# Performance work log

Hardware: AMD Instinct MI355X
Metric: run time of the kernel (lower is better)

The kernel has to match this reference:

```python
import jax, jax.numpy as jnp
import numpy as np

EPS = 1e-5
TEMPERATURE = 1.0


def _gn(x, w, b):
    # GroupNorm(dim, dim): num_groups == channels -> per-channel norm over spatial
    mu = x.mean((2, 3), keepdims=True)
    var = x.var((2, 3), keepdims=True)
    return (x - mu) * jax.lax.rsqrt(var + EPS) * w[None, :, None, None] + b[None, :, None, None]


def _deconv(x, w, b):
    # torch ConvTranspose2d(Cin, Cout, 3, stride=2, padding=1, output_padding=1)
    # == dilated conv with lhs_dilation=2, padding (1,2); kernel flip absorbed into random weights
    y = jax.lax.conv_general_dilated(
        x, w, window_strides=(1, 1), padding=((1, 2), (1, 2)),
        lhs_dilation=(2, 2), dimension_numbers=('NCHW', 'OIHW', 'NCHW'))
    return y + b[None, :, None, None]


def _spatial_softmax(logits, temp):
    # logits (..., h, w) -> expected (x, y) coords in [-1, 1], shape (..., 2)
    h, w = logits.shape[-2], logits.shape[-1]
    p = jax.nn.softmax(logits.reshape(*logits.shape[:-2], h * w) / temp, axis=-1)
    ys, xs = jnp.meshgrid(jnp.linspace(-1.0, 1.0, h), jnp.linspace(-1.0, 1.0, w), indexing='ij')
    ex = p @ xs.reshape(-1)
    ey = p @ ys.reshape(-1)
    return jnp.stack([ex, ey], axis=-1)


def setup_inputs() -> dict:
    key = jax.random.key(0)
    ks = iter(jax.random.split(key, 40))
    B, FC, FH = 512, 256, 4   # batch, encoder channels, encoder spatial
    H = 512                   # hidden_size
    STEPS, NHEADS, C = 5, 3, H // 8

    def nrm(shape, scale):
        return jax.random.normal(next(ks), shape, jnp.float32) * scale

    inp = {
        'feat': nrm((B, FC, FH, FH), 1.0),
        'action': jax.random.randint(next(ks), (B,), 0, NHEADS),
        'scene_idx': jax.random.randint(next(ks), (B,), 0, 10),
        'fc_w': nrm((FC, H), (2.0 / FC) ** 0.5),
        'fc_b': jnp.zeros((H,), jnp.float32),
    }
    for i, d in enumerate([512, 256, 128]):
        inp[f'gw{i}'] = jnp.ones((d,), jnp.float32)
        inp[f'gb{i}'] = jnp.zeros((d,), jnp.float32)
        inp[f'dw{i}'] = nrm((d // 2, d, 3, 3), (2.0 / (d * 9)) ** 0.5)
        inp[f'db{i}'] = jnp.zeros((d // 2,), jnp.float32)
    inp['hgw'] = jnp.ones((NHEADS, C), jnp.float32)
    inp['hgb'] = jnp.zeros((NHEADS, C), jnp.float32)
    inp['hcw'] = nrm((NHEADS, STEPS, C), (2.0 / C) ** 0.5)
    inp['hcb'] = jnp.zeros((NHEADS, STEPS), jnp.float32)
    return inp


def reference(feat, action, scene_idx, fc_w, fc_b,
              gw0, gb0, dw0, db0, gw1, gb1, dw1, db1, gw2, gb2, dw2, db2,
              hgw, hgb, hcw, hcb):
    # visual_fc1 applied channel-last == 1x1 linear over channels
    x = jax.nn.relu(jnp.einsum('bchw,cd->bdhw', feat, fc_w) + fc_b[None, :, None, None])
    # deconv stack: (B,512,4,4) -> (B,256,8,8) -> (B,128,16,16) -> (B,64,32,32)
    for gw, gb, dw, db in ((gw0, gb0, dw0, db0), (gw1, gb1, dw1, db1), (gw2, gb2, dw2, db2)):
        x = jax.nn.relu(_deconv(_gn(x, gw, gb), dw, db))
    # expert heads: shared per-channel normalization, head-specific affine fused into 1x1 conv
    mu = x.mean((2, 3), keepdims=True)
    var = x.var((2, 3), keepdims=True)
    xn = (x - mu) * jax.lax.rsqrt(var + EPS)                       # (B,64,32,32)
    w_eff = hcw * hgw[:, None, :]                                  # (A,S,C)
    b_eff = hcb + jnp.einsum('asc,ac->as', hcw, hgb)               # (A,S)
    logits = jnp.einsum('bchw,asc->abshw', xn, w_eff) + b_eff[:, None, :, None, None]
    coords = _spatial_softmax(logits, TEMPERATURE)                 # (A,B,S,2)
    # route each sample to its action's head (== masked scatter loop in torch)
    out = coords[action, jnp.arange(action.shape[0])]              # (B,S,2)
    return out
```

## Files before the change

kernel.cpp:

```cpp
#include <hip/hip_runtime.h>
#include <hip/hip_bf16.h>

#define DI __device__ __forceinline__
using u16 = unsigned short;
using u32 = unsigned int;

typedef short short8 __attribute__((ext_vector_type(8)));
typedef float f32x4 __attribute__((ext_vector_type(4)));

#define F4C(v, i) ((i) == 0 ? (v).x : (i) == 1 ? (v).y : (i) == 2 ? (v).z : (v).w)

DI float bflo(u32 u) { return __uint_as_float(u << 16); }
DI float bfhi(u32 u) { return __uint_as_float(u & 0xffff0000u); }
DI float bfel(uint2 u, int j) { u32 w = (j < 2) ? u.x : u.y; return (j & 1) ? bfhi(w) : bflo(w); }
DI u16 f2bf(float a) {
  u32 xu = __float_as_uint(a);
  return (u16)((xu + 0x7fffu + ((xu >> 16) & 1)) >> 16);
}
DI u32 pack_bf16x2(float a, float b) {
  u32 xu = __float_as_uint(a), yu = __float_as_uint(b);
  xu = (xu + 0x7fffu + ((xu >> 16) & 1)) >> 16;
  yu = (yu + 0x7fffu + ((yu >> 16) & 1)) >> 16;
  return (xu & 0xffffu) | (yu << 16);
}

static constexpr size_t OFF_REGB = 0;
static constexpr size_t OFF_REGA = 16777216;
static constexpr size_t OFF_WT0  = 33554432;
static constexpr size_t OFF_WT1  = OFF_WT0 + 1179648;
static constexpr size_t OFF_WT2  = OFF_WT1 + 294912;
static constexpr size_t OFF_WTF  = OFF_WT2 + 73728;
static constexpr size_t OFF_ST   = 35200000;
static constexpr size_t O_SC0 = OFF_ST,          O_SH0 = OFF_ST + 262144;
static constexpr size_t O_SC1 = OFF_ST + 524288, O_SH1 = OFF_ST + 655360;
static constexpr size_t O_SC2 = OFF_ST + 786432, O_SH2 = OFF_ST + 851968;
static constexpr size_t O_PSUM = OFF_ST + 1048576;

__global__ __launch_bounds__(256)
void wtrans_all(const float* __restrict__ dw0, const float* __restrict__ dw1,
                const float* __restrict__ dw2, const float* __restrict__ fcw,
                u16* __restrict__ wt0, u16* __restrict__ wt1,
                u16* __restrict__ wt2, u16* __restrict__ wtf)
{
  int id = blockIdx.x * 256 + threadIdx.x;
  if (id < 131072) {
    int m = id >> 9, c = id & 511;
    const float* src = dw0 + ((size_t)m * 512 + c) * 9;
#pragma unroll
    for (int tap = 0; tap < 9; ++tap)
      wt0[((size_t)tap * 256 + m) * 512 + c] = f2bf(src[tap]);
  } else if (id < 163840) {
    int j = id - 131072;
    int m = j >> 8, c = j & 255;
    const float* src = dw1 + ((size_t)m * 256 + c) * 9;
#pragma unroll
    for (int tap = 0; tap < 9; ++tap)
      wt1[((size_t)tap * 128 + m) * 256 + c] = f2bf(src[tap]);
  } else if (id < 172032) {
    int j = id - 163840;
    int m = j >> 7, c = j & 127;
    const float* src = dw2 + ((size_t)m * 128 + c) * 9;
#pragma unroll
    for (int tap = 0; tap < 9; ++tap)
      wt2[((size_t)tap * 64 + m) * 128 + c] = f2bf(src[tap]);
  } else {
    int j = id - 172032;
    int d = j >> 8, c = j & 255;
    wtf[j] = f2bf(fcw[c * 512 + d]);
  }
}

DI void fc_stage_A(const float* __restrict__ feat, int b, u16* Ab, int t)
{
#pragma unroll
  for (int it = 0; it < 2; ++it) {
    int idx = t + it * 256;
    int cp = idx >> 2, hw4 = idx & 3;
    int c = cp * 2;
    const float* xp = feat + ((size_t)b * 256 + c) * 16 + hw4 * 4;
    float4 v0 = *(const float4*)xp;
    float4 v1 = *(const float4*)(xp + 16);
    int c64 = c >> 6, jb = (c & 63) >> 3;
#pragma unroll
    for (int j = 0; j < 4; ++j) {
      int hw = hw4 * 4 + j;
      int row = c64 * 16 + hw;
      *(u32*)&Ab[(row << 6) + ((jb ^ (row & 7)) << 3) + (c & 7)] =
          pack_bf16x2(F4C(v0, j), F4C(v1, j));
    }
  }
}

__global__ __launch_bounds__(256, 2)
void fc_mfma(const float* __restrict__ feat, const u16* __restrict__ wtf,
             const float* __restrict__ fb, const float* __restrict__ gw,
             const float* __restrict__ gb, u16* __restrict__ x0,
             float* __restrict__ sc, float* __restrict__ sh)
{
  __shared__ __align__(16) u16 Wl[256 * 64];
  __shared__ __align__(16) u16 Al[2][64 * 64];
  const int t = threadIdx.x;
  const int lane = t & 63, wave = t >> 6;
  const int n15 = lane & 15, kq = lane >> 4;
  const int d0 = blockIdx.x * 64;
  const int b0 = blockIdx.y * 4;

#pragma unroll
  for (int it = 0; it < 8; ++it) {
    int idx = t + it * 256;
    int dl = idx >> 5, jb32 = idx & 31;
    int row = (jb32 >> 3) * 64 + dl, jb = jb32 & 7;
    uint4 v = *(const uint4*)(wtf + (size_t)(d0 + dl) * 256 + jb32 * 8);
    *(uint4*)&Wl[(row << 6) + ((jb ^ (row & 7)) << 3)] = v;
  }
  fc_stage_A(feat, b0, Al[0], t);

  const int dg = d0 + wave * 16 + n15;
  const float bvn = fb[dg];
  const float gwv = gw[dg], gbv = gb[dg];

  for (int bi = 0; bi < 4; ++bi) {
    __syncthreads();
    if (bi + 1 < 4) fc_stage_A(feat, b0 + bi + 1, Al[(bi + 1) & 1], t);

    const u16* A = Al[bi & 1];
    f32x4 acc0 = {0.f, 0.f, 0.f, 0.f}, acc1 = {0.f, 0.f, 0.f, 0.f};
#pragma unroll
    for (int ks = 0; ks < 8; ++ks) {
      int js = ks * 4 + kq;
      int ra = (js >> 3) * 16 + n15;
      int rb = (js >> 3) * 64 + wave * 16 + n15;
      short8 av = *(const short8*)&A[(ra << 6) + (((js & 7) ^ (ra & 7)) << 3)];
      short8 bv = *(const short8*)&Wl[(rb << 6) + (((js & 7) ^ (rb & 7)) << 3)];
      if (ks & 1) acc1 = __builtin_amdgcn_mfma_f32_16x16x32_bf16(av, bv, acc1, 0, 0, 0);
      else        acc0 = __builtin_amdgcn_mfma_f32_16x16x32_bf16(av, bv, acc0, 0, 0, 0);
    }

    int b = b0 + bi;
    float v[4], s = 0.f, s2 = 0.f;
#pragma unroll
    for (int r = 0; r < 4; ++r) {
      v[r] = fmaxf(acc0[r] + acc1[r] + bvn, 0.f);
      s += v[r]; s2 += v[r] * v[r];
    }
    uint2 pk = {pack_bf16x2(v[0], v[1]), pack_bf16x2(v[2], v[3])};
    *(uint2*)&x0[((size_t)b * 512 + dg) * 16 + kq * 4] = pk;
    s  += __shfl_xor(s, 16, 64);  s  += __shfl_xor(s, 32, 64);
    s2 += __shfl_xor(s2, 16, 64); s2 += __shfl_xor(s2, 32, 64);
    if (kq == 0) {
      float mu = s * (1.f / 16.f);
      float var = fmaxf(s2 * (1.f / 16.f) - mu * mu, 0.f);
      float scale = gwv * rsqrtf(var + 1e-5f);
      sc[(size_t)b * 512 + dg] = scale;
      sh[(size_t)b * 512 + dg] = gbv - mu * scale;
    }
  }
}

template<int STAGE>
__global__ __launch_bounds__(256, 3)
void deconv_mfma(const u16* __restrict__ x, const float* __restrict__ sc,
                 const float* __restrict__ sh, const u16* __restrict__ wt,
                 const float* __restrict__ bias, u16* __restrict__ y,
                 const float* __restrict__ gwn, const float* __restrict__ gbn,
                 float* __restrict__ osc, float* __restrict__ osh)
{
  constexpr int CI  = STAGE == 0 ? 512 : 256;
  constexpr int CO  = CI / 2;
  constexpr int H   = STAGE == 0 ? 4 : 8;
  constexpr int S2I = H * H, S2O = 4 * S2I, W2 = 2 * H;
  constexpr int WP  = H + 1;
  constexpr int XROWS = STAGE == 0 ? 100 : 81;
  constexpr int NCH = CI / 64;
  __shared__ __align__(16) u16 Wl[288 * 64];
  __shared__ __align__(16) u16 Xl[XROWS * 64];
  __shared__ float2 sbuf[4][32];

  const int t = threadIdx.x;
  const int lane = t & 63, wv = t >> 6;
  const int n15 = lane & 15, kq = lane >> 4;

  const int m0 = blockIdx.x * 32;
  const int b0 = (STAGE == 0) ? blockIdx.y * 4 : blockIdx.y;
  const int b  = (STAGE == 0) ? b0 + wv : b0;

  int xrow;
  if constexpr (STAGE == 0) xrow = wv * 25 + (n15 >> 2) * 5 + (n15 & 3);
  else                      xrow = (2 * wv + (n15 >> 3)) * 9 + (n15 & 7);

  for (int i = t; i < XROWS * 32; i += 256) ((u32*)Xl)[i] = 0;

  f32x4 acc[2][4];
#pragma unroll
  for (int mi = 0; mi < 2; ++mi)
#pragma unroll
    for (int c = 0; c < 4; ++c) acc[mi][c] = f32x4{0.f, 0.f, 0.f, 0.f};

  for (int ch = 0; ch < NCH; ++ch) {
    const int c0 = ch * 64;
    __syncthreads();

#pragma unroll
    for (int it = 0; it < 9; ++it) {
      int idx = t + it * 256;
      int row = idx >> 3, jb = idx & 7;
      int tap = row >> 5, ml = row & 31;
      uint4 v = *(const uint4*)(wt + ((size_t)(tap * CO + m0 + ml)) * CI + c0 + jb * 8);
      *(uint4*)&Wl[(row << 6) + ((jb ^ (row & 7)) << 3)] = v;
    }

    for (int idx = t; idx < 16 * 32; idx += 256) {
      int q = idx & 15, p = idx >> 4;
      int c = c0 + 2 * p;
      int bb, ldr, gpos;
      if constexpr (STAGE == 0) {
        int img = q >> 2, iy = q & 3;
        bb = b0 + img; gpos = iy * 4; ldr = img * 25 + iy * 5;
      } else {
        int iy = q >> 1, cq = q & 1;
        bb = b0; gpos = iy * 8 + cq * 4; ldr = iy * 9 + cq * 4;
      }
      const u16* xp = x + ((size_t)bb * CI + c) * S2I + gpos;
      uint2 q0 = *(const uint2*)xp;
      uint2 q1 = *(const uint2*)(xp + S2I);
      float s0 = sc[(size_t)bb * CI + c],     h0 = sh[(size_t)bb * CI + c];
      float s1 = sc[(size_t)bb * CI + c + 1], h1 = sh[(size_t)bb * CI + c + 1];
      int jb = p >> 2, sub = p & 3;
#pragma unroll
      for (int j = 0; j < 4; ++j) {
        int row = ldr + j;
        *(u32*)&Xl[(row << 6) + ((jb ^ (row & 7)) << 3) + sub * 2] =
            pack_bf16x2(bfel(q0, j) * s0 + h0, bfel(q1, j) * s1 + h1);
      }
    }
    __syncthreads();

#pragma unroll
    for (int s = 0; s < 2; ++s) {
      const int js = s * 4 + kq;
      const int r0 = xrow, r1 = r0 + 1, r2 = r0 + WP, r3 = r0 + WP + 1;
      short8 b00 = *(const short8*)&Xl[(r0 << 6) + ((js ^ (r0 & 7)) << 3)];
      short8 b01 = *(const short8*)&Xl[(r1 << 6) + ((js ^ (r1 & 7)) << 3)];
      short8 b10 = *(const short8*)&Xl[(r2 << 6) + ((js ^ (r2 & 7)) << 3)];
      short8 b11 = *(const short8*)&Xl[(r3 << 6) + ((js ^ (r3 & 7)) << 3)];
#pragma unroll
      for (int mi = 0; mi < 2; ++mi) {
        short8 a[9];
#pragma unroll
        for (int tap = 0; tap < 9; ++tap) {
          int row = tap * 32 + mi * 16 + n15;
          a[tap] = *(const short8*)&Wl[(row << 6) + ((js ^ (row & 7)) << 3)];
        }
        acc[mi][0] = __builtin_amdgcn_mfma_f32_16x16x32_bf16(a[4], b00, acc[mi][0], 0, 0, 0);
        acc[mi][1] = __builtin_amdgcn_mfma_f32_16x16x32_bf16(a[3], b00, acc[mi][1], 0, 0, 0);
        acc[mi][1] = __builtin_amdgcn_mfma_f32_16x16x32_bf16(a[5], b01, acc[mi][1], 0, 0, 0);
        acc[mi][2] = __builtin_amdgcn_mfma_f32_16x16x32_bf16(a[1], b00, acc[mi][2], 0, 0, 0);
        acc[mi][2] = __builtin_amdgcn_mfma_f32_16x16x32_bf16(a[7], b10, acc[mi][2], 0, 0, 0);
        acc[mi][3] = __builtin_amdgcn_mfma_f32_16x16x32_bf16(a[0], b00, acc[mi][3], 0, 0, 0);
        acc[mi][3] = __builtin_amdgcn_mfma_f32_16x16x32_bf16(a[2], b01, acc[mi][3], 0, 0, 0);
        acc[mi][3] = __builtin_amdgcn_mfma_f32_16x16x32_bf16(a[6], b10, acc[mi][3], 0, 0, 0);
        acc[mi][3] = __builtin_amdgcn_mfma_f32_16x16x32_bf16(a[8], b11, acc[mi][3], 0, 0, 0);
      }
    }
  }

#pragma unroll
  for (int mi = 0; mi < 2; ++mi) {
    float bvv[4];
#pragma unroll
    for (int r = 0; r < 4; ++r) bvv[r] = bias[m0 + mi * 16 + kq * 4 + r];
    float val[4][4];
    float sr[4] = {0.f, 0.f, 0.f, 0.f}, sr2[4] = {0.f, 0.f, 0.f, 0.f};
#pragma unroll
    for (int cl = 0; cl < 4; ++cl)
#pragma unroll
      for (int r = 0; r < 4; ++r) {
        val[cl][r] = fmaxf(acc[mi][cl][r] + bvv[r], 0.f);
        sr[r] += val[cl][r]; sr2[r] += val[cl][r] * val[cl][r];
      }

    if constexpr (STAGE == 0) {
      int iy = n15 >> 2, ix = n15 & 3;
#pragma unroll
      for (int r = 0; r < 4; ++r) {
        int m = m0 + mi * 16 + kq * 4 + r;
        size_t base = ((size_t)b * CO + m) * S2O + (size_t)(2 * iy) * W2 + 2 * ix;
        *(u32*)(y + base)      = pack_bf16x2(val[0][r], val[1][r]);
        *(u32*)(y + base + W2) = pack_bf16x2(val[2][r], val[3][r]);
      }
#pragma unroll
      for (int r = 0; r < 4; ++r) {
#pragma unroll
        for (int off = 1; off <= 8; off <<= 1) {
          sr[r]  += __shfl_xor(sr[r], off, 64);
          sr2[r] += __shfl_xor(sr2[r], off, 64);
        }
      }
      if (n15 == 0) {
#pragma unroll
        for (int r = 0; r < 4; ++r) {
          int m = m0 + mi * 16 + kq * 4 + r;
          float mu = sr[r] * (1.f / 64.f);
          float var = fmaxf(sr2[r] * (1.f / 64.f) - mu * mu, 0.f);
          float scale = gwn[m] * rsqrtf(var + 1e-5f);
          osc[(size_t)b * CO + m] = scale;
          osh[(size_t)b * CO + m] = gbn[m] - mu * scale;
        }
      }
    } else {
      int iy = 2 * wv + (n15 >> 3), ix = n15 & 7;
#pragma unroll
      for (int cl = 0; cl < 4; ++cl) {
        int opx = (2 * iy + (cl >> 1)) * 16 + 2 * ix + (cl & 1);
        size_t base = ((size_t)b * 256 + opx) * 128 + m0 + mi * 16 + kq * 4;
        *(u32*)(y + base)     = pack_bf16x2(val[cl][0], val[cl][1]);
        *(u32*)(y + base + 2) = pack_bf16x2(val[cl][2], val[cl][3]);
      }
#pragma unroll
      for (int r = 0; r < 4; ++r) {
#pragma unroll
        for (int off = 1; off <= 8; off <<= 1) {
          sr[r]  += __shfl_xor(sr[r], off, 64);
          sr2[r] += __shfl_xor(sr2[r], off, 64);
        }
      }
      if (n15 == 0) {
#pragma unroll
        for (int r = 0; r < 4; ++r) sbuf[wv][mi * 16 + kq * 4 + r] = float2{sr[r], sr2[r]};
      }
    }
  }

  if constexpr (STAGE == 1) {
    __syncthreads();
    if (t < 32) {
      float s = 0.f, s2 = 0.f;
#pragma unroll
      for (int w = 0; w < 4; ++w) { s += sbuf[w][t].x; s2 += sbuf[w][t].y; }
      float mu = s * (1.f / 256.f);
      float var = fmaxf(s2 * (1.f / 256.f) - mu * mu, 0.f);
      int m = m0 + t;
      float scale = gwn[m] * rsqrtf(var + 1e-5f);
      osc[(size_t)b0 * CO + m] = scale;
      osh[(size_t)b0 * CO + m] = gbn[m] - mu * scale;
    }
  }
}

#define XRD(row) (*(const short8*)&Xl[((row) << 6) + (((js ^ ((row) & 7))) << 3)])
__global__ __launch_bounds__(256, 3)
void deconv2_q(const u16* __restrict__ x, const float* __restrict__ sc,
               const float* __restrict__ sh, const u16* __restrict__ wt,
               const float* __restrict__ bias, u16* __restrict__ y,
               float2* __restrict__ psum)
{
  __shared__ __align__(16) u16 Wl[288 * 64];
  __shared__ __align__(16) u16 Xl[85 * 64];
  __shared__ float sc_l[128], sh_l[128];
  __shared__ float2 sbuf[2][2][16];

  const int t = threadIdx.x;
  const int lane = t & 63, wave = t >> 6;
  const int ms = wave >> 1, ns = wave & 1;
  const int n15 = lane & 15, kq = lane >> 4;
  const int m0 = (blockIdx.x & 1) * 32;
  const int qz = blockIdx.x >> 1;
  const int b  = blockIdx.y;

  if (t < 128) { sc_l[t] = sc[(size_t)b * 128 + t]; sh_l[t] = sh[(size_t)b * 128 + t]; }
  for (int i = t; i < 85 * 32; i += 256) ((u32*)Xl)[i] = 0;

  const int am = ms * 16 + n15;
  const int xr0 = (ns * 2) * 17 + n15;

  f32x4 acc[2][4];
#pragma unroll
  for (int ni = 0; ni < 2; ++ni)
#pragma unroll
    for (int c = 0; c < 4; ++c) acc[ni][c] = f32x4{0.f, 0.f, 0.f, 0.f};

  const int NPX = (qz < 3) ? 80 : 64;
  for (int ch = 0; ch < 2; ++ch) {
    const int c0 = ch * 64;
    __syncthreads();

#pragma unroll
    for (int it = 0; it < 9; ++it) {
      int idx = t + it * 256;
      int row = idx >> 3, jb = idx & 7;
      int tap = row >> 5, ml = row & 31;
      uint4 v = *(const uint4*)(wt + ((size_t)(tap * 64 + m0 + ml)) * 128 + c0 + jb * 8);
      *(uint4*)&Wl[(row << 6) + ((jb ^ (row & 7)) << 3)] = v;
    }

    for (int idx = t; idx < NPX * 8; idx += 256) {
      int pxl = idx >> 3, jb = idx & 7;
      int rl = pxl >> 4, ix = pxl & 15;
      int gpx = (4 * qz + rl) * 16 + ix;
      uint4 q = *(const uint4*)(x + ((size_t)b * 256 + gpx) * 128 + c0 + jb * 8);
      int cb = c0 + jb * 8;
      float f0 = bflo(q.x) * sc_l[cb + 0] + sh_l[cb + 0];
      float f1 = bfhi(q.x) * sc_l[cb + 1] + sh_l[cb + 1];
      float f2 = bflo(q.y) * sc_l[cb + 2] + sh_l[cb + 2];
      float f3 = bfhi(q.y) * sc_l[cb + 3] + sh_l[cb + 3];
      float f4 = bflo(q.z) * sc_l[cb + 4] + sh_l[cb + 4];
      float f5 = bfhi(q.z) * sc_l[cb + 5] + sh_l[cb + 5];
      float f6 = bflo(q.w) * sc_l[cb + 6] + sh_l[cb + 6];
      float f7 = bfhi(q.w) * sc_l[cb + 7] + sh_l[cb + 7];
      uint4 o = {pack_bf16x2(f0, f1), pack_bf16x2(f2, f3),
                 pack_bf16x2(f4, f5), pack_bf16x2(f6, f7)};
      int row = rl * 17 + ix;
      *(uint4*)&Xl[(row << 6) + ((jb ^ (row & 7)) << 3)] = o;
    }
    __syncthreads();

#pragma unroll
    for (int s = 0; s < 2; ++s) {
      const int js = s * 4 + kq;
      short8 a[9];
#pragma unroll
      for (int tap = 0; tap < 9; ++tap) {
        int row = tap * 32 + am;
        a[tap] = *(const short8*)&Wl[(row << 6) + ((js ^ (row & 7)) << 3)];
      }
      short8 B0 = XRD(xr0),      B1 = XRD(xr0 + 1);
      short8 B2 = XRD(xr0 + 17), B3 = XRD(xr0 + 18);
      short8 B4 = XRD(xr0 + 34), B5 = XRD(xr0 + 35);
#pragma unroll
      for (int ni = 0; ni < 2; ++ni) {
        short8 b00 = ni ? B2 : B0, b01 = ni ? B3 : B1;
        short8 b10 = ni ? B4 : B2, b11 = ni ? B5 : B3;
        acc[ni][0] = __builtin_amdgcn_mfma_f32_16x16x32_bf16(a[4], b00, acc[ni][0], 0, 0, 0);
        acc[ni][1] = __builtin_amdgcn_mfma_f32_16x16x32_bf16(a[3], b00, acc[ni][1], 0, 0, 0);
        acc[ni][1] = __builtin_amdgcn_mfma_f32_16x16x32_bf16(a[5], b01, acc[ni][1], 0, 0, 0);
        acc[ni][2] = __builtin_amdgcn_mfma_f32_16x16x32_bf16(a[1], b00, acc[ni][2], 0, 0, 0);
        acc[ni][2] = __builtin_amdgcn_mfma_f32_16x16x32_bf16(a[7], b10, acc[ni][2], 0, 0, 0);
        acc[ni][3] = __builtin_amdgcn_mfma_f32_16x16x32_bf16(a[0], b00, acc[ni][3], 0, 0, 0);
        acc[ni][3] = __builtin_amdgcn_mfma_f32_16x16x32_bf16(a[2], b01, acc[ni][3], 0, 0, 0);
        acc[ni][3] = __builtin_amdgcn_mfma_f32_16x16x32_bf16(a[6], b10, acc[ni][3], 0, 0, 0);
        acc[ni][3] = __builtin_amdgcn_mfma_f32_16x16x32_bf16(a[8], b11, acc[ni][3], 0, 0, 0);
      }
    }
  }

  float bv[4];
#pragma unroll
  for (int r = 0; r < 4; ++r) bv[r] = bias[m0 + ms * 16 + kq * 4 + r];
  float sr[4] = {0.f, 0.f, 0.f, 0.f}, sr2[4] = {0.f, 0.f, 0.f, 0.f};
#pragma unroll
  for (int ni = 0; ni < 2; ++ni) {
    int iy = 4 * qz + ns * 2 + ni, ix = n15;
#pragma unroll
    for (int r = 0; r < 4; ++r) {
      int m = m0 + ms * 16 + kq * 4 + r;
      float v00 = fmaxf(acc[ni][0][r] + bv[r], 0.f);
      float v01 = fmaxf(acc[ni][1][r] + bv[r], 0.f);
      float v10 = fmaxf(acc[ni][2][r] + bv[r], 0.f);
      float v11 = fmaxf(acc[ni][3][r] + bv[r], 0.f);
      size_t base = ((size_t)b * 64 + m) * 1024 + (size_t)(2 * iy) * 32 + 2 * ix;
      *(u32*)(y + base)      = pack_bf16x2(v00, v01);
      *(u32*)(y + base + 32) = pack_bf16x2(v10, v11);
      sr[r]  += v00 + v01 + v10 + v11;
      sr2[r] += v00 * v00 + v01 * v01 + v10 * v10 + v11 * v11;
    }
  }
#pragma unroll
  for (int r = 0; r < 4; ++r) {
#pragma unroll
    for (int off = 1; off <= 8; off <<= 1) {
      sr[r]  += __shfl_xor(sr[r], off, 64);
      sr2[r] += __shfl_xor(sr2[r], off, 64);
    }
  }
  __syncthreads();
  if (n15 == 0) {
#pragma unroll
    for (int r = 0; r < 4; ++r) sbuf[ms][ns][kq * 4 + r] = float2{sr[r], sr2[r]};
  }
  __syncthreads();
  if (t < 32) {
    int msx = t >> 4, i = t & 15;
    float2 p0 = sbuf[msx][0][i], p1 = sbuf[msx][1][i];
    int m = m0 + msx * 16 + i;
    psum[((size_t)b * 64 + m) * 4 + qz] = float2{p0.x + p1.x, p0.y + p1.y};
  }
}

DI float breduce_sum(float v, float* buf) {
#pragma unroll
  for (int off = 32; off; off >>= 1) v += __shfl_xor(v, off, 64);
  if ((threadIdx.x & 63) == 0) buf[threadIdx.x >> 6] = v;
  __syncthreads();
  float r = (buf[0] + buf[1]) + (buf[2] + buf[3]);
  __syncthreads();
  return r;
}
DI float breduce_max(float v, float* buf) {
#pragma unroll
  for (int off = 32; off; off >>= 1) v = fmaxf(v, __shfl_xor(v, off, 64));
  if ((threadIdx.x & 63) == 0) buf[threadIdx.x >> 6] = v;
  __syncthreads();
  float r = fmaxf(fmaxf(buf[0], buf[1]), fmaxf(buf[2], buf[3]));
  __syncthreads();
  return r;
}

__global__ __launch_bounds__(256)
void head_kernel(const u16* __restrict__ x3, const float2* __restrict__ psum,
                 const int* __restrict__ action, const float* __restrict__ hgw,
                 const float* __restrict__ hcw, float* __restrict__ out)
{
  constexpr int C = 64, S = 5, P = 1024;
  const int b = blockIdx.x, t = threadIdx.x;
  const int a = action[b];
  __shared__ float weff[S * C];
  __shared__ float sc_l[C], sh_l[C];
  __shared__ float rbuf[4];
  if (t < C) {
    float s = 0.f, s2 = 0.f;
#pragma unroll
    for (int qz = 0; qz < 4; ++qz) {
      float2 p = psum[((size_t)b * C + t) * 4 + qz];
      s += p.x; s2 += p.y;
    }
    float mu = s * (1.f / 1024.f);
    float var = fmaxf(s2 * (1.f / 1024.f) - mu * mu, 0.f);
    float rstd = rsqrtf(var + 1e-5f);
    sc_l[t] = rstd; sh_l[t] = -mu * rstd;
  }
  for (int j = t; j < S * C; j += 256) {
    int s = j >> 6, c = j & 63;
    weff[j] = hcw[(a * S + s) * C + c] * hgw[a * C + c];
  }
  __syncthreads();

  float L[S][4];
#pragma unroll
  for (int s = 0; s < S; ++s)
#pragma unroll
    for (int k = 0; k < 4; ++k) L[s][k] = 0.f;

  const u32* xb = (const u32*)(x3 + (size_t)b * C * P);
  for (int c = 0; c < C; ++c) {
    float scv = sc_l[c], shv = sh_l[c];
    u32 u0 = xb[c * 512 + t];
    u32 u1 = xb[c * 512 + t + 256];
    float xv[4] = {bflo(u0) * scv + shv, bfhi(u0) * scv + shv,
                   bflo(u1) * scv + shv, bfhi(u1) * scv + shv};
#pragma unroll
    for (int s = 0; s < S; ++s) {
      float wv = weff[s * C + c];
#pragma unroll
      for (int k = 0; k < 4; ++k) L[s][k] += xv[k] * wv;
    }
  }

#pragma unroll
  for (int s = 0; s < S; ++s) {
    float m = fmaxf(fmaxf(L[s][0], L[s][1]), fmaxf(L[s][2], L[s][3]));
    m = breduce_max(m, rbuf);
    float se = 0.f, sx = 0.f, sy = 0.f;
    const int pix[4] = {2 * t, 2 * t + 1, 512 + 2 * t, 512 + 2 * t + 1};
#pragma unroll
    for (int k = 0; k < 4; ++k) {
      int p = pix[k];
      float e = __expf(L[s][k] - m);
      se += e;
      sx += e * ((float)(p & 31) * (2.f / 31.f) - 1.f);
      sy += e * ((float)(p >> 5) * (2.f / 31.f) - 1.f);
    }
    se = breduce_sum(se, rbuf);
    sx = breduce_sum(sx, rbuf);
    sy = breduce_sum(sy, rbuf);
    if (t == 0) {
      out[(b * S + s) * 2 + 0] = sx / se;
      out[(b * S + s) * 2 + 1] = sy / se;
    }
  }
}

extern "C" void kernel_launch(void* const* d_in, const int* in_sizes, int n_in,
                              void* d_out, int out_size, void* d_ws, size_t ws_size,
                              hipStream_t stream)
{
  (void)in_sizes; (void)n_in; (void)out_size; (void)ws_size;
  const float* feat   = (const float*)d_in[0];
  const int*   action = (const int*)d_in[1];
  const float* fc_w = (const float*)d_in[3];
  const float* fc_b = (const float*)d_in[4];
  const float* gw0  = (const float*)d_in[5];
  const float* gb0  = (const float*)d_in[6];
  const float* dw0  = (const float*)d_in[7];
  const float* db0  = (const float*)d_in[8];
  const float* gw1  = (const float*)d_in[9];
  const float* gb1  = (const float*)d_in[10];
  const float* dw1  = (const float*)d_in[11];
  const float* db1  = (const float*)d_in[12];
  const float* gw2  = (const float*)d_in[13];
  const float* gb2  = (const float*)d_in[14];
  const float* dw2  = (const float*)d_in[15];
  const float* db2  = (const float*)d_in[16];
  const float* hgw  = (const float*)d_in[17];
  const float* hcw  = (const float*)d_in[19];

  float* ws = (float*)d_ws;
  u16* x0 = (u16*)(ws + OFF_REGB);
  u16* x2 = (u16*)(ws + OFF_REGB);
  u16* x1 = (u16*)(ws + OFF_REGA);
  u16* x3 = (u16*)(ws + OFF_REGA);
  u16* wt0 = (u16*)(ws + OFF_WT0);
  u16* wt1 = (u16*)(ws + OFF_WT1);
  u16* wt2 = (u16*)(ws + OFF_WT2);
  u16* wtf = (u16*)(ws + OFF_WTF);
  float* sc0 = ws + O_SC0; float* sh0 = ws + O_SH0;
  float* sc1 = ws + O_SC1; float* sh1 = ws + O_SH1;
  float* sc2 = ws + O_SC2; float* sh2 = ws + O_SH2;
  float2* psum = (float2*)(ws + O_PSUM);

  wtrans_all<<<1184, 256, 0, stream>>>(dw0, dw1, dw2, fc_w, wt0, wt1, wt2, wtf);
  fc_mfma<<<dim3(8, 128), 256, 0, stream>>>(feat, wtf, fc_b, gw0, gb0, x0, sc0, sh0);
  deconv_mfma<0><<<dim3(8, 128), 256, 0, stream>>>(x0, sc0, sh0, wt0, db0, x1, gw1, gb1, sc1, sh1);
  deconv_mfma<1><<<dim3(4, 512), 256, 0, stream>>>(x1, sc1, sh1, wt1, db1, x2, gw2, gb2, sc2, sh2);
  deconv2_q<<<dim3(8, 512), 256, 0, stream>>>(x2, sc2, sh2, wt2, db2, x3, psum);
  head_kernel<<<512, 256, 0, stream>>>(x3, psum, action, hgw, hcw, (float*)d_out);
}
```

Before: 268.4 us.

## Retile last deconv to half-image blocks with 32-channel K slices

The final deconv kernel now gives each block half the image (8 input rows) instead of a quarter (4 rows), and halves the grid to 4x512. Each wave computes 4 row tiles, and consecutive rows share B fragments through a sliding-window register reuse. The input halo overhead per output falls and weight tiles are loaded half as many times across the grid. The channel loop runs in four 32-channel slices with a new 4-way swizzled LDS layout, so LDS use shrinks, but there are twice as many sync points and more accumulator registers (16 f32x4), which could affect occupancy under launch_bounds(256,3). The psum partial-stat layout changes from 4 to 2 partials per channel, and the head kernel is updated to match.

```diff
diff --git a/kernel.cpp b/kernel.cpp
--- a/kernel.cpp
+++ b/kernel.cpp
@@ -347,15 +347,16 @@
   }
 }
 
-#define XRD(row) (*(const short8*)&Xl[((row) << 6) + (((js ^ ((row) & 7))) << 3)])
+#define PIX(row, jb) (((((row) >> 1)) << 6) + (((row) & 1) << 5) + ((((jb) ^ (((row) >> 1) & 3))) << 3))
+#define XR2(row) (*(const short8*)&Xl[PIX(row, kq)])
 __global__ __launch_bounds__(256, 3)
-void deconv2_q(const u16* __restrict__ x, const float* __restrict__ sc,
-               const float* __restrict__ sh, const u16* __restrict__ wt,
-               const float* __restrict__ bias, u16* __restrict__ y,
-               float2* __restrict__ psum)
+void deconv2_hs(const u16* __restrict__ x, const float* __restrict__ sc,
+                const float* __restrict__ sh, const u16* __restrict__ wt,
+                const float* __restrict__ bias, u16* __restrict__ y,
+                float2* __restrict__ psum)
 {
-  __shared__ __align__(16) u16 Wl[288 * 64];
-  __shared__ __align__(16) u16 Xl[85 * 64];
+  __shared__ __align__(16) u16 Wl[144 * 64];
+  __shared__ __align__(16) u16 Xl[77 * 64];
   __shared__ float sc_l[128], sh_l[128];
   __shared__ float2 sbuf[2][2][16];
 
@@ -364,39 +365,37 @@
   const int ms = wave >> 1, ns = wave & 1;
   const int n15 = lane & 15, kq = lane >> 4;
   const int m0 = (blockIdx.x & 1) * 32;
-  const int qz = blockIdx.x >> 1;
+  const int h  = blockIdx.x >> 1;
   const int b  = blockIdx.y;
 
   if (t < 128) { sc_l[t] = sc[(size_t)b * 128 + t]; sh_l[t] = sh[(size_t)b * 128 + t]; }
-  for (int i = t; i < 85 * 32; i += 256) ((u32*)Xl)[i] = 0;
-
-  const int am = ms * 16 + n15;
-  const int xr0 = (ns * 2) * 17 + n15;
-
-  f32x4 acc[2][4];
-#pragma unroll
-  for (int ni = 0; ni < 2; ++ni)
-#pragma unroll
-    for (int c = 0; c < 4; ++c) acc[ni][c] = f32x4{0.f, 0.f, 0.f, 0.f};
-
-  const int NPX = (qz < 3) ? 80 : 64;
-  for (int ch = 0; ch < 2; ++ch) {
-    const int c0 = ch * 64;
+  for (int i = t; i < 77 * 32; i += 256) ((u32*)Xl)[i] = 0;
+
+  f32x4 acc[4][4];
+#pragma unroll
+  for (int n = 0; n < 4; ++n)
+#pragma unroll
+    for (int c = 0; c < 4; ++c) acc[n][c] = f32x4{0.f, 0.f, 0.f, 0.f};
+
+  const int NPX = (h == 0) ? 144 : 128;
+  for (int cs = 0; cs < 4; ++cs) {
+    const int c0 = cs * 32;
     __syncthreads();
 
 #pragma unroll
-    for (int it = 0; it < 9; ++it) {
+    for (int it = 0; it < 5; ++it) {
       int idx = t + it * 256;
-      int row = idx >> 3, jb = idx & 7;
-      int tap = row >> 5, ml = row & 31;
-      uint4 v = *(const uint4*)(wt + ((size_t)(tap * 64 + m0 + ml)) * 128 + c0 + jb * 8);
-      *(uint4*)&Wl[(row << 6) + ((jb ^ (row & 7)) << 3)] = v;
-    }
-
-    for (int idx = t; idx < NPX * 8; idx += 256) {
-      int pxl = idx >> 3, jb = idx & 7;
-      int rl = pxl >> 4, ix = pxl & 15;
-      int gpx = (4 * qz + rl) * 16 + ix;
+      if (idx < 1152) {
+        int row = idx >> 2, jb = idx & 3;
+        int tap = row >> 5, ml = row & 31;
+        uint4 v = *(const uint4*)(wt + ((size_t)(tap * 64 + m0 + ml)) * 128 + c0 + jb * 8);
+        *(uint4*)&Wl[PIX(row, jb)] = v;
+      }
+    }
+
+    for (int idx = t; idx < NPX * 4; idx += 256) {
+      int pxl = idx >> 2, jb = idx & 3;
+      int gpx = h * 128 + pxl;
       uint4 q = *(const uint4*)(x + ((size_t)b * 256 + gpx) * 128 + c0 + jb * 8);
       int cb = c0 + jb * 8;
       float f0 = bflo(q.x) * sc_l[cb + 0] + sh_l[cb + 0];
@@ -409,37 +408,33 @@
       float f7 = bfhi(q.w) * sc_l[cb + 7] + sh_l[cb + 7];
       uint4 o = {pack_bf16x2(f0, f1), pack_bf16x2(f2, f3),
                  pack_bf16x2(f4, f5), pack_bf16x2(f6, f7)};
+      int rl = pxl >> 4, ix = pxl & 15;
       int row = rl * 17 + ix;
-      *(uint4*)&Xl[(row << 6) + ((jb ^ (row & 7)) << 3)] = o;
+      *(uint4*)&Xl[PIX(row, jb)] = o;
     }
     __syncthreads();
 
-#pragma unroll
-    for (int s = 0; s < 2; ++s) {
-      const int js = s * 4 + kq;
-      short8 a[9];
-#pragma unroll
-      for (int tap = 0; tap < 9; ++tap) {
-        int row = tap * 32 + am;
-        a[tap] = *(const short8*)&Wl[(row << 6) + ((js ^ (row & 7)) << 3)];
-      }
-      short8 B0 = XRD(xr0),      B1 = XRD(xr0 + 1);
-      short8 B2 = XRD(xr0 + 17), B3 = XRD(xr0 + 18);
-      short8 B4 = XRD(xr0 + 34), B5 = XRD(xr0 + 35);
-#pragma unroll
-      for (int ni = 0; ni < 2; ++ni) {
-        short8 b00 = ni ? B2 : B0, b01 = ni ? B3 : B1;
-        short8 b10 = ni ? B4 : B2, b11 = ni ? B5 : B3;
-        acc[ni][0] = __builtin_amdgcn_mfma_f32_16x16x32_bf16(a[4], b00, acc[ni][0], 0, 0, 0);
-        acc[ni][1] = __builtin_amdgcn_mfma_f32_16x16x32_bf16(a[3], b00, acc[ni][1], 0, 0, 0);
-        acc[ni][1] = __builtin_amdgcn_mfma_f32_16x16x32_bf16(a[5], b01, acc[ni][1], 0, 0, 0);
-        acc[ni][2] = __builtin_amdgcn_mfma_f32_16x16x32_bf16(a[1], b00, acc[ni][2], 0, 0, 0);
-        acc[ni][2] = __builtin_amdgcn_mfma_f32_16x16x32_bf16(a[7], b10, acc[ni][2], 0, 0, 0);
-        acc[ni][3] = __builtin_amdgcn_mfma_f32_16x16x32_bf16(a[0], b00, acc[ni][3], 0, 0, 0);
-        acc[ni][3] = __builtin_amdgcn_mfma_f32_16x16x32_bf16(a[2], b01, acc[ni][3], 0, 0, 0);
-        acc[ni][3] = __builtin_amdgcn_mfma_f32_16x16x32_bf16(a[6], b10, acc[ni][3], 0, 0, 0);
-        acc[ni][3] = __builtin_amdgcn_mfma_f32_16x16x32_bf16(a[8], b11, acc[ni][3], 0, 0, 0);
-      }
+    short8 a[9];
+#pragma unroll
+    for (int tap = 0; tap < 9; ++tap) {
+      int row = tap * 32 + ms * 16 + n15;
+      a[tap] = *(const short8*)&Wl[PIX(row, kq)];
+    }
+    int r = (ns * 4) * 17 + n15;
+    short8 b00 = XR2(r), b01 = XR2(r + 1);
+#pragma unroll
+    for (int nt = 0; nt < 4; ++nt) {
+      short8 b10 = XR2(r + 17), b11 = XR2(r + 18);
+      acc[nt][0] = __builtin_amdgcn_mfma_f32_16x16x32_bf16(a[4], b00, acc[nt][0], 0, 0, 0);
+      acc[nt][1] = __builtin_amdgcn_mfma_f32_16x16x32_bf16(a[3], b00, acc[nt][1], 0, 0, 0);
+      acc[nt][1] = __builtin_amdgcn_mfma_f32_16x16x32_bf16(a[5], b01, acc[nt][1], 0, 0, 0);
+      acc[nt][2] = __builtin_amdgcn_mfma_f32_16x16x32_bf16(a[1], b00, acc[nt][2], 0, 0, 0);
+      acc[nt][2] = __builtin_amdgcn_mfma_f32_16x16x32_bf16(a[7], b10, acc[nt][2], 0, 0, 0);
+      acc[nt][3] = __builtin_amdgcn_mfma_f32_16x16x32_bf16(a[0], b00, acc[nt][3], 0, 0, 0);
+      acc[nt][3] = __builtin_amdgcn_mfma_f32_16x16x32_bf16(a[2], b01, acc[nt][3], 0, 0, 0);
+      acc[nt][3] = __builtin_amdgcn_mfma_f32_16x16x32_bf16(a[6], b10, acc[nt][3], 0, 0, 0);
+      acc[nt][3] = __builtin_amdgcn_mfma_f32_16x16x32_bf16(a[8], b11, acc[nt][3], 0, 0, 0);
+      b00 = b10; b01 = b11; r += 17;
     }
   }
 
@@ -448,15 +443,15 @@
   for (int r = 0; r < 4; ++r) bv[r] = bias[m0 + ms * 16 + kq * 4 + r];
   float sr[4] = {0.f, 0.f, 0.f, 0.f}, sr2[4] = {0.f, 0.f, 0.f, 0.f};
 #pragma unroll
-  for (int ni = 0; ni < 2; ++ni) {
-    int iy = 4 * qz + ns * 2 + ni, ix = n15;
+  for (int nt = 0; nt < 4; ++nt) {
+    int iy = h * 8 + ns * 4 + nt, ix = n15;
 #pragma unroll
     for (int r = 0; r < 4; ++r) {
       int m = m0 + ms * 16 + kq * 4 + r;
-      float v00 = fmaxf(acc[ni][0][r] + bv[r], 0.f);
-      float v01 = fmaxf(acc[ni][1][r] + bv[r], 0.f);
-      float v10 = fmaxf(acc[ni][2][r] + bv[r], 0.f);
-      float v11 = fmaxf(acc[ni][3][r] + bv[r], 0.f);
+      float v00 = fmaxf(acc[nt][0][r] + bv[r], 0.f);
+      float v01 = fmaxf(acc[nt][1][r] + bv[r], 0.f);
+      float v10 = fmaxf(acc[nt][2][r] + bv[r], 0.f);
+      float v11 = fmaxf(acc[nt][3][r] + bv[r], 0.f);
       size_t base = ((size_t)b * 64 + m) * 1024 + (size_t)(2 * iy) * 32 + 2 * ix;
       *(u32*)(y + base)      = pack_bf16x2(v00, v01);
       *(u32*)(y + base + 32) = pack_bf16x2(v10, v11);
@@ -482,7 +477,7 @@
     int msx = t >> 4, i = t & 15;
     float2 p0 = sbuf[msx][0][i], p1 = sbuf[msx][1][i];
     int m = m0 + msx * 16 + i;
-    psum[((size_t)b * 64 + m) * 4 + qz] = float2{p0.x + p1.x, p0.y + p1.y};
+    psum[((size_t)b * 64 + m) * 2 + h] = float2{p0.x + p1.x, p0.y + p1.y};
   }
 }
 
@@ -517,12 +512,9 @@
   __shared__ float sc_l[C], sh_l[C];
   __shared__ float rbuf[4];
   if (t < C) {
-    float s = 0.f, s2 = 0.f;
-#pragma unroll
-    for (int qz = 0; qz < 4; ++qz) {
-      float2 p = psum[((size_t)b * C + t) * 4 + qz];
-      s += p.x; s2 += p.y;
-    }
+    float2 p0 = psum[((size_t)b * C + t) * 2 + 0];
+    float2 p1 = psum[((size_t)b * C + t) * 2 + 1];
+    float s = p0.x + p1.x, s2 = p0.y + p1.y;
     float mu = s * (1.f / 1024.f);
     float var = fmaxf(s2 * (1.f / 1024.f) - mu * mu, 0.f);
     float rstd = rsqrtf(var + 1e-5f);
@@ -621,6 +613,6 @@
   fc_mfma<<<dim3(8, 128), 256, 0, stream>>>(feat, wtf, fc_b, gw0, gb0, x0, sc0, sh0);
   deconv_mfma<0><<<dim3(8, 128), 256, 0, stream>>>(x0, sc0, sh0, wt0, db0, x1, gw1, gb1, sc1, sh1);
   deconv_mfma<1><<<dim3(4, 512), 256, 0, stream>>>(x1, sc1, sh1, wt1, db1, x2, gw2, gb2, sc2, sh2);
-  deconv2_q<<<dim3(8, 512), 256, 0, stream>>>(x2, sc2, sh2, wt2, db2, x3, psum);
+  deconv2_hs<<<dim3(4, 512), 256, 0, stream>>>(x2, sc2, sh2, wt2, db2, x3, psum);
   head_kernel<<<512, 256, 0, stream>>>(x3, psum, action, hgw, hcw, (float*)d_out);
 }
```

After: 272.7 us. No clear change (+1.6%).
